# Optimization experiments

Hardware: AMD Instinct MI355X
Metric: run time of the kernel (lower is better)

Reference implementation:

```python
import jax, jax.numpy as jnp
import numpy as np

WS = 7       # window_size
SHIFT = 3    # shift_size
HEADS = 3
EPS = 1e-5


def _rel_index():
    # (2, N) coords of a WS x WS window, then pairwise relative offsets -> flat table index
    coords = np.stack(np.meshgrid(np.arange(WS), np.arange(WS), indexing='ij')).reshape(2, -1)
    rel = (coords[:, :, None] - coords[:, None, :]).transpose(1, 2, 0) + (WS - 1)  # (N,N,2)
    return jnp.asarray(rel[..., 0] * (2 * WS - 1) + rel[..., 1])  # (N,N) int


def _layernorm(x, g, b):
    mu = jnp.mean(x, axis=-1, keepdims=True)
    var = jnp.mean(jnp.square(x - mu), axis=-1, keepdims=True)
    return (x - mu) * jax.lax.rsqrt(var + EPS) * g + b


def setup_inputs() -> dict:
    key = jax.random.key(0)
    ks = jax.random.split(key, 6)
    C, HID = 96, 384
    s = 0.02
    return {
        'x': jax.random.normal(ks[0], (8, C, 224, 224), jnp.float32),
        'norm1_g': jnp.ones((C,), jnp.float32),
        'norm1_b': jnp.zeros((C,), jnp.float32),
        'qkv_w': jax.random.normal(ks[1], (C, 3 * C), jnp.float32) * s,
        'qkv_b': jnp.zeros((3 * C,), jnp.float32),
        'proj_w': jax.random.normal(ks[2], (C, C), jnp.float32) * s,
        'proj_b': jnp.zeros((C,), jnp.float32),
        'rel_bias_table': jax.random.normal(ks[3], ((2 * WS - 1) ** 2, HEADS), jnp.float32) * s,
        'norm2_g': jnp.ones((C,), jnp.float32),
        'norm2_b': jnp.zeros((C,), jnp.float32),
        'fc1_w': jax.random.normal(ks[4], (C, HID), jnp.float32) * s,
        'fc1_b': jnp.zeros((HID,), jnp.float32),
        'fc2_w': jax.random.normal(ks[5], (HID, C), jnp.float32) * s,
        'fc2_b': jnp.zeros((C,), jnp.float32),
    }


def reference(x, norm1_g, norm1_b, qkv_w, qkv_b, proj_w, proj_b,
              rel_bias_table, norm2_g, norm2_b, fc1_w, fc1_b, fc2_w, fc2_b):
    B, C, H, W = x.shape
    N = WS * WS
    dh = C // HEADS

    # norm1 over channels (tokens = flattened spatial)
    xt = x.reshape(B, C, H * W).transpose(0, 2, 1)          # (B, L, C)
    xn = _layernorm(xt, norm1_g, norm1_b)
    xs = xn.transpose(0, 2, 1).reshape(B, C, H, W)
    # H, W divisible by WS -> pad is a no-op; cyclic shift
    xs = jnp.roll(xs, (-SHIFT, -SHIFT), axis=(2, 3))

    # window partition -> (B*nW, N, C)
    xw = xs.reshape(B, C, H // WS, WS, W // WS, WS)
    xw = xw.transpose(0, 2, 4, 3, 5, 1).reshape(-1, N, C)

    # window attention with relative position bias (no shift mask, per source)
    Bw = xw.shape[0]
    qkv = (xw @ qkv_w + qkv_b).reshape(Bw, N, 3, HEADS, dh).transpose(2, 0, 3, 1, 4)
    q, k, v = qkv[0], qkv[1], qkv[2]                        # (Bw, h, N, dh)
    attn = jnp.einsum('bhnd,bhmd->bhnm', q, k) * (dh ** -0.5)
    bias = rel_bias_table[_rel_index().reshape(-1)].reshape(N, N, HEADS).transpose(2, 0, 1)
    attn = jax.nn.softmax(attn + bias, axis=-1)
    out = jnp.einsum('bhnm,bhmd->bhnd', attn, v).transpose(0, 2, 1, 3).reshape(Bw, N, C)
    out = out @ proj_w + proj_b

    # window reverse + unshift
    xr = out.reshape(B, H // WS, W // WS, WS, WS, C)
    xr = xr.transpose(0, 5, 1, 3, 2, 4).reshape(B, C, H, W)
    xr = jnp.roll(xr, (SHIFT, SHIFT), axis=(2, 3))

    x = x + xr                                              # residual 1

    # MLP branch with norm2 (exact GELU, matching torch nn.GELU default)
    xt = x.reshape(B, C, H * W).transpose(0, 2, 1)
    xn = _layernorm(xt, norm2_g, norm2_b)
    h = jax.nn.gelu(xn @ fc1_w + fc1_b, approximate=False)
    h = h @ fc2_w + fc2_b
    return x + h.transpose(0, 2, 1).reshape(B, C, H, W)
```

## Files before the change

### kernel.cpp

```cpp
#include <hip/hip_runtime.h>
#include <hip/hip_bf16.h>
#include <math.h>

#define WSZ 7
#define NTOK 49
#define CH 96
#define HIMG 224
#define WIMG 224
#define HWIMG (224*224)
#define SHIFT_ 3
#define HID 384

typedef __attribute__((ext_vector_type(8))) short bf16x8;
typedef __attribute__((ext_vector_type(4))) float f32x4;
typedef unsigned int u32;
typedef unsigned short u16;

__device__ __forceinline__ u32 pk2(float a, float b) {
    u16 ua = __builtin_bit_cast(u16, __float2bfloat16(a));
    u16 ub = __builtin_bit_cast(u16, __float2bfloat16(b));
    return (u32)ua | ((u32)ub << 16);
}
__device__ __forceinline__ float bflo(u32 u) { return __builtin_bit_cast(float, u << 16); }
__device__ __forceinline__ float bfhi(u32 u) { return __builtin_bit_cast(float, u & 0xFFFF0000u); }

union FragU { u32 w[4]; bf16x8 v; };

__device__ __forceinline__ bf16x8 regroup(u32 t0w0, u32 t0w1, u32 t1w0, u32 t1w1, int lane) {
    int sl0 = (lane & 15) + ((lane & 16) << 1);
    int sl1 = sl0 + 16;
    u32 x0 = (u32)__shfl((int)t0w0, sl0);
    u32 y0 = (u32)__shfl((int)t1w0, sl0);
    u32 x1 = (u32)__shfl((int)t0w1, sl0);
    u32 y1 = (u32)__shfl((int)t1w1, sl0);
    u32 x2 = (u32)__shfl((int)t0w0, sl1);
    u32 y2 = (u32)__shfl((int)t1w0, sl1);
    u32 x3 = (u32)__shfl((int)t0w1, sl1);
    u32 y3 = (u32)__shfl((int)t1w1, sl1);
    bool lo = lane < 32;
    FragU f;
    f.w[0] = lo ? x0 : y0;
    f.w[1] = lo ? x1 : y1;
    f.w[2] = lo ? x2 : y2;
    f.w[3] = lo ? x3 : y3;
    return f.v;
}

__device__ __forceinline__ float gelu_f(float x) {
    float x2 = x * x;
    float t  = x * (1.5957691216057308f + 0.07135481283587191f * x2);
    float e  = __expf(t);
    float r  = __builtin_amdgcn_rcpf(e + 1.0f);
    return x - x * r;
}

__global__ __launch_bounds__(256) void prep_kernel(
    const float* __restrict__ w1, const float* __restrict__ w2,
    const float* __restrict__ pw, const float* __restrict__ qw,
    __hip_bfloat16* __restrict__ ws, int n)
{
    int i = blockIdx.x * 256 + threadIdx.x;
    if (i >= n) return;
    float val = 0.f;
    if (i < 81920) {
        int ch = i / 20480, r = i - ch * 20480;
        int half = r / 10240;
        int rr = r - half * 10240;
        if (rr < 9984) {
            int row = rr / 104, col = rr - row * 104;
            if (col < 96)
                val = (half == 0) ? w1[col * HID + ch * 96 + row]
                                  : w2[(size_t)(ch * 96 + col) * CH + row];
        }
    } else if (i < 92160) {
        int r = i - 81920;
        if (r < 9984) {
            int row = r / 104, col = r - row * 104;
            if (col < 96) val = pw[col * CH + row];
        }
    } else {
        int j = i - 92160;
        int hh = j / 9984, rr = j - hh * 9984;
        int dp = rr / 104, c = rr - dp * 104;
        if (c < 96) {
            int colW = (dp < 32) ? (hh * 32 + dp)
                     : (dp < 64) ? (96 + hh * 32 + dp - 32)
                                 : (192 + hh * 32 + dp - 64);
            val = qw[c * 288 + colW];
        }
    }
    ws[i] = __float2bfloat16(val);
}

__global__ __launch_bounds__(256) void attn2_kernel(
    const float* __restrict__ x,
    const float* __restrict__ g1, const float* __restrict__ b1,
    const __hip_bfloat16* __restrict__ wsW,
    const float* __restrict__ qkv_b, const float* __restrict__ pb,
    const float* __restrict__ btab,
    __hip_bfloat16* __restrict__ projout)
{
    const int tid  = threadIdx.x;
    const int lane = tid & 63;
    const int wv   = tid >> 6;
    const int l15  = lane & 15;
    const int g    = lane >> 4;
    const int bi   = blockIdx.x;
    const int b    = bi >> 8;
    const int wh   = (bi >> 3) & 31;
    const int ww0  = (bi & 7) * 4;
    const int ww   = ww0 + wv;

    __shared__ float btabL[512];
    __shared__ __align__(16) __hip_bfloat16 slab[32][7][32];
    __shared__ __align__(16) char uniA[4][4608];

    __hip_bfloat16 (*vT)[72] = (__hip_bfloat16(*)[72])uniA[wv];
    u32* prS = (u32*)uniA[wv];

    for (int idx = tid; idx < 507; idx += 256) btabL[idx] = btab[idx];

    const int colBase = ww0 * 7 + 3;
    const int cb4 = (colBase & ~3) >> 2;
    const int a0  = colBase & 3;

    int yiA[4], scA[4]; bool realA[4];
    #pragma unroll
    for (int it = 0; it < 4; ++it) {
        int i = it * 16 + l15;
        realA[it] = i < NTOK;
        int yi = i / 7, xi = i - yi * 7;
        yiA[it] = yi; scA[it] = a0 + wv * 7 + xi;
    }

    float s0a[4] = {0.f, 0.f, 0.f, 0.f}, s1a[4] = {0.f, 0.f, 0.f, 0.f};
    FragU xf[4][3];

    for (int ks = 0; ks < 3; ++ks) {
        #pragma unroll
        for (int k = 0; k < 7; ++k) {
            int idx = tid + 256 * k;
            int c = idx / 56, rem = idx - c * 56;
            int r = rem >> 3, cf = rem & 7;
            int gr = wh * 7 + 3 + r; if (gr >= HIMG) gr -= HIMG;
            int g4 = cb4 + cf; if (g4 >= 56) g4 -= 56;
            float4 v = *(const float4*)(x + ((size_t)(b * CH + ks * 32 + c) * HIMG + gr) * WIMG + g4 * 4);
            uint2 pk;
            pk.x = pk2(v.x, v.y);
            pk.y = pk2(v.z, v.w);
            *(uint2*)&slab[c][r][cf * 4] = pk;
        }
        __syncthreads();
        #pragma unroll
        for (int it = 0; it < 4; ++it) {
            float v[8];
            #pragma unroll
            for (int t = 0; t < 8; ++t) {
                float val = realA[it] ? __bfloat162float(slab[g * 8 + t][yiA[it]][scA[it]]) : 0.f;
                v[t] = val;
                s0a[it] += val; s1a[it] += val * val;
            }
            xf[it][ks].w[0] = pk2(v[0], v[1]);
            xf[it][ks].w[1] = pk2(v[2], v[3]);
            xf[it][ks].w[2] = pk2(v[4], v[5]);
            xf[it][ks].w[3] = pk2(v[6], v[7]);
        }
        __syncthreads();
    }

    float mu4[4], rs4[4];
    #pragma unroll
    for (int it = 0; it < 4; ++it) {
        float s0 = s0a[it]; s0 += __shfl_xor(s0, 16); s0 += __shfl_xor(s0, 32);
        float s1 = s1a[it]; s1 += __shfl_xor(s1, 16); s1 += __shfl_xor(s1, 32);
        float mu = s0 * (1.0f / CH);
        mu4[it] = mu;
        rs4[it] = rsqrtf(s1 * (1.0f / CH) - mu * mu + 1e-5f);
    }
    #pragma unroll
    for (int ks = 0; ks < 3; ++ks) {
        float4 gA = *(const float4*)&g1[ks * 32 + g * 8];
        float4 gB = *(const float4*)&g1[ks * 32 + g * 8 + 4];
        float4 bA = *(const float4*)&b1[ks * 32 + g * 8];
        float4 bB = *(const float4*)&b1[ks * 32 + g * 8 + 4];
        float gg[8] = {gA.x, gA.y, gA.z, gA.w, gB.x, gB.y, gB.z, gB.w};
        float bb[8] = {bA.x, bA.y, bA.z, bA.w, bB.x, bB.y, bB.z, bB.w};
        #pragma unroll
        for (int it = 0; it < 4; ++it) {
            #pragma unroll
            for (int w = 0; w < 4; ++w) {
                u32 u = xf[it][ks].w[w];
                float lo = bflo(u), hi = bfhi(u);
                float nlo = realA[it] ? ((lo - mu4[it]) * rs4[it] * gg[2 * w]     + bb[2 * w])     : 0.f;
                float nhi = realA[it] ? ((hi - mu4[it]) * rs4[it] * gg[2 * w + 1] + bb[2 * w + 1]) : 0.f;
                xf[it][ks].w[w] = pk2(nlo, nhi);
            }
        }
    }

    const float scale = 0.17677669529663687f;
    bf16x8 aoB[3][4];

    for (int h = 0; h < 3; ++h) {
        const __hip_bfloat16* qkvTg = wsW + 92160 + h * 9984;

        float qb[2][4], kb[2][4], vb[2][4];
        #pragma unroll
        for (int dt = 0; dt < 2; ++dt)
            #pragma unroll
            for (int r = 0; r < 4; ++r) {
                int d = h * 32 + dt * 16 + g * 4 + r;
                qb[dt][r] = qkv_b[d];
                kb[dt][r] = qkv_b[96 + d];
                vb[dt][r] = qkv_b[192 + d];
            }

        u32 Qpk[2][4][2];
        #pragma unroll
        for (int dt = 0; dt < 2; ++dt) {
            const __hip_bfloat16* wr = qkvTg + (dt * 16 + l15) * 104 + g * 8;
            bf16x8 a0f = *(const bf16x8*)(wr);
            bf16x8 a1f = *(const bf16x8*)(wr + 32);
            bf16x8 a2f = *(const bf16x8*)(wr + 64);
            #pragma unroll
            for (int it = 0; it < 4; ++it) {
                f32x4 c4 = {0.f, 0.f, 0.f, 0.f};
                c4 = __builtin_amdgcn_mfma_f32_16x16x32_bf16(a0f, xf[it][0].v, c4, 0, 0, 0);
                c4 = __builtin_amdgcn_mfma_f32_16x16x32_bf16(a1f, xf[it][1].v, c4, 0, 0, 0);
                c4 = __builtin_amdgcn_mfma_f32_16x16x32_bf16(a2f, xf[it][2].v, c4, 0, 0, 0);
                Qpk[dt][it][0] = pk2(c4[0] + qb[dt][0], c4[1] + qb[dt][1]);
                Qpk[dt][it][1] = pk2(c4[2] + qb[dt][2], c4[3] + qb[dt][3]);
            }
        }
        bf16x8 QB[4];
        #pragma unroll
        for (int it = 0; it < 4; ++it)
            QB[it] = regroup(Qpk[0][it][0], Qpk[0][it][1], Qpk[1][it][0], Qpk[1][it][1], lane);

        u32 Kpk[2][4][2];
        #pragma unroll
        for (int dt = 0; dt < 2; ++dt) {
            const __hip_bfloat16* wr = qkvTg + (32 + dt * 16 + l15) * 104 + g * 8;
            bf16x8 a0f = *(const bf16x8*)(wr);
            bf16x8 a1f = *(const bf16x8*)(wr + 32);
            bf16x8 a2f = *(const bf16x8*)(wr + 64);
            #pragma unroll
            for (int it = 0; it < 4; ++it) {
                f32x4 c4 = {0.f, 0.f, 0.f, 0.f};
                c4 = __builtin_amdgcn_mfma_f32_16x16x32_bf16(a0f, xf[it][0].v, c4, 0, 0, 0);
                c4 = __builtin_amdgcn_mfma_f32_16x16x32_bf16(a1f, xf[it][1].v, c4, 0, 0, 0);
                c4 = __builtin_amdgcn_mfma_f32_16x16x32_bf16(a2f, xf[it][2].v, c4, 0, 0, 0);
                Kpk[dt][it][0] = pk2(c4[0] + kb[dt][0], c4[1] + kb[dt][1]);
                Kpk[dt][it][1] = pk2(c4[2] + kb[dt][2], c4[3] + kb[dt][3]);
            }
        }
        bf16x8 KA[4];
        #pragma unroll
        for (int it = 0; it < 4; ++it)
            KA[it] = regroup(Kpk[0][it][0], Kpk[0][it][1], Kpk[1][it][0], Kpk[1][it][1], lane);

        #pragma unroll
        for (int dt = 0; dt < 2; ++dt) {
            const __hip_bfloat16* wr = qkvTg + (64 + dt * 16 + l15) * 104 + g * 8;
            bf16x8 a0f = *(const bf16x8*)(wr);
            bf16x8 a1f = *(const bf16x8*)(wr + 32);
            bf16x8 a2f = *(const bf16x8*)(wr + 64);
            #pragma unroll
            for (int it = 0; it < 4; ++it) {
                f32x4 c4 = {0.f, 0.f, 0.f, 0.f};
                c4 = __builtin_amdgcn_mfma_f32_16x16x32_bf16(a0f, xf[it][0].v, c4, 0, 0, 0);
                c4 = __builtin_amdgcn_mfma_f32_16x16x32_bf16(a1f, xf[it][1].v, c4, 0, 0, 0);
                c4 = __builtin_amdgcn_mfma_f32_16x16x32_bf16(a2f, xf[it][2].v, c4, 0, 0, 0);
                #pragma unroll
                for (int r = 0; r < 4; ++r)
                    vT[dt * 16 + g * 4 + r][it * 16 + l15] = __float2bfloat16(c4[r] + vb[dt][r]);
            }
        }
        bf16x8 VBf[2][2];
        #pragma unroll
        for (int dt = 0; dt < 2; ++dt)
            #pragma unroll
            for (int ks = 0; ks < 2; ++ks)
                VBf[dt][ks] = *(const bf16x8*)&vT[dt * 16 + l15][ks * 32 + g * 8];

        #pragma unroll
        for (int it = 0; it < 4; ++it) {
            f32x4 SC[4];
            #pragma unroll
            for (int jt = 0; jt < 4; ++jt) {
                f32x4 z = {0.f, 0.f, 0.f, 0.f};
                SC[jt] = __builtin_amdgcn_mfma_f32_16x16x32_bf16(KA[jt], QB[it], z, 0, 0, 0);
            }
            int i = it * 16 + l15;
            int yi = i / 7, xi = i - yi * 7;
            float p[16];
            float m = -1e30f;
            #pragma unroll
            for (int jt = 0; jt < 4; ++jt)
                #pragma unroll
                for (int r = 0; r < 4; ++r) {
                    int j = jt * 16 + g * 4 + r;
                    int yj = j / 7, xj = j - yj * 7;
                    int rel = (yi - yj + 6) * 13 + (xi - xj + 6);
                    rel = rel < 0 ? 0 : (rel > 168 ? 168 : rel);
                    float s = (j < NTOK) ? (SC[jt][r] * scale + btabL[rel * 3 + h]) : -1e30f;
                    p[jt * 4 + r] = s;
                    m = fmaxf(m, s);
                }
            m = fmaxf(m, __shfl_xor(m, 16));
            m = fmaxf(m, __shfl_xor(m, 32));
            float sum = 0.f;
            #pragma unroll
            for (int q = 0; q < 16; ++q) { float e = __expf(p[q] - m); p[q] = e; sum += e; }
            sum += __shfl_xor(sum, 16);
            sum += __shfl_xor(sum, 32);
            float inv = 1.f / sum;
            u32 Ppk[4][2];
            #pragma unroll
            for (int jt = 0; jt < 4; ++jt) {
                Ppk[jt][0] = pk2(p[jt * 4 + 0] * inv, p[jt * 4 + 1] * inv);
                Ppk[jt][1] = pk2(p[jt * 4 + 2] * inv, p[jt * 4 + 3] * inv);
            }
            bf16x8 PA0 = regroup(Ppk[0][0], Ppk[0][1], Ppk[1][0], Ppk[1][1], lane);
            bf16x8 PA1 = regroup(Ppk[2][0], Ppk[2][1], Ppk[3][0], Ppk[3][1], lane);
            u32 opk[2][2];
            #pragma unroll
            for (int dt = 0; dt < 2; ++dt) {
                f32x4 o = {0.f, 0.f, 0.f, 0.f};
                o = __builtin_amdgcn_mfma_f32_16x16x32_bf16(PA0, VBf[dt][0], o, 0, 0, 0);
                o = __builtin_amdgcn_mfma_f32_16x16x32_bf16(PA1, VBf[dt][1], o, 0, 0, 0);
                opk[dt][0] = pk2(o[0], o[1]);
                opk[dt][1] = pk2(o[2], o[3]);
            }
            aoB[h][it] = regroup(opk[0][0], opk[0][1], opk[1][0], opk[1][1], lane);
        }
    }

    const __hip_bfloat16* pwTg = wsW + 81920;
    for (int it = 0; it < 4; ++it) {
        #pragma unroll
        for (int mt = 0; mt < 6; ++mt) {
            const __hip_bfloat16* wr = pwTg + (mt * 16 + l15) * 104 + g * 8;
            f32x4 cp = {0.f, 0.f, 0.f, 0.f};
            #pragma unroll
            for (int ks = 0; ks < 3; ++ks) {
                bf16x8 af = *(const bf16x8*)(wr + ks * 32);
                cp = __builtin_amdgcn_mfma_f32_16x16x32_bf16(af, aoB[ks][it], cp, 0, 0, 0);
            }
            float v0 = cp[0] + pb[mt * 16 + g * 4 + 0];
            float v1 = cp[1] + pb[mt * 16 + g * 4 + 1];
            float v2 = cp[2] + pb[mt * 16 + g * 4 + 2];
            float v3 = cp[3] + pb[mt * 16 + g * 4 + 3];
            prS[l15 * 52 + mt * 8 + g * 2 + 0] = pk2(v0, v1);
            prS[l15 * 52 + mt * 8 + g * 2 + 1] = pk2(v2, v3);
        }
        #pragma unroll
        for (int s = 0; s < 3; ++s) {
            int chunk = lane + 64 * s;
            int row = chunk / 12, q = chunk - row * 12;
            int tok = it * 16 + row;
            if (tok < NTOK) {
                int yi = tok / 7, xi = tok - yi * 7;
                int hh = wh * 7 + yi + SHIFT_; if (hh >= HIMG) hh -= HIMG;
                int wp = ww * 7 + xi + SHIFT_; if (wp >= WIMG) wp -= WIMG;
                float4 val = *(const float4*)((const char*)prS + row * 208 + q * 16);
                *(float4*)(projout + ((size_t)b * HWIMG + hh * WIMG + wp) * 96 + q * 8) = val;
            }
        }
    }
}

#define LDSTG(p0, p1, p2, s) { const float4* _s = wsrc + (s) * 1280; \
    p0 = _s[tid]; p1 = _s[tid + 512]; if (tid < 256) p2 = _s[tid + 1024]; }
#define WRSTG(p0, p1, p2, off) { float4* _d = (float4*)(SB + (off)); \
    _d[tid] = p0; _d[tid + 512] = p1; if (tid < 256) _d[tid + 1024] = p2; }

__global__ __launch_bounds__(512, 4) void mlp2_kernel(
    const float* __restrict__ x, const __hip_bfloat16* __restrict__ projout,
    const float* __restrict__ g2, const float* __restrict__ b2,
    const float* __restrict__ bb1, const float* __restrict__ bb2,
    const __hip_bfloat16* __restrict__ wsW,
    float* __restrict__ out)
{
    const int tid = threadIdx.x;
    const int lane = tid & 63, wv = tid >> 6;
    const int l15 = lane & 15, g = lane >> 4;
    const int b = blockIdx.x / 392;
    const int hw0 = (blockIdx.x % 392) * 128;
    const int tok = wv * 16 + l15;

    __shared__ __align__(16) char SB[50688];
    __shared__ float bb1S[HID];

    __hip_bfloat16 (*xnS)[104] = (__hip_bfloat16(*)[104])SB;
    __hip_bfloat16 (*wT0)[104] = (__hip_bfloat16(*)[104])SB;
    __hip_bfloat16 (*wT1)[104] = (__hip_bfloat16(*)[104])(SB + 20480);
    float* ob = (float*)SB;

    const float4* wsrc = (const float4*)wsW;
    float4 ra0, ra1, ra2, rb0, rb1, rb2;

    LDSTG(ra0, ra1, ra2, 0);

    #pragma unroll
    for (int s = 0; s < 3; ++s) {
        int chunk = tid + 512 * s;
        int row = chunk / 12, q = chunk - row * 12;
        *(float4*)&xnS[row][q * 8] =
            *(const float4*)(projout + ((size_t)b * HWIMG + hw0 + row) * 96 + q * 8);
    }
    for (int idx = tid; idx < HID; idx += 512) bb1S[idx] = bb1[idx];
    __syncthreads();

    float xr[24];
    float s0 = 0.f, s1 = 0.f;
    bf16x8 pf[3];
    #pragma unroll
    for (int ks = 0; ks < 3; ++ks)
        pf[ks] = *(const bf16x8*)&xnS[tok][ks * 32 + g * 8];
    const float* xb = x + (size_t)(b * CH) * HWIMG + hw0 + tok;
    #pragma unroll
    for (int ks = 0; ks < 3; ++ks)
        #pragma unroll
        for (int j = 0; j < 8; ++j) {
            int c = ks * 32 + g * 8 + j;
            float xv = xb[(size_t)c * HWIMG];
            float v = xv + bflo((u32)(u16)pf[ks][j]);
            xr[ks * 8 + j] = v; s0 += v; s1 += v * v;
        }
    s0 += __shfl_xor(s0, 16); s0 += __shfl_xor(s0, 32);
    s1 += __shfl_xor(s1, 16); s1 += __shfl_xor(s1, 32);
    float mu = s0 * (1.0f / CH);
    float rstd = rsqrtf(s1 * (1.0f / CH) - mu * mu + 1e-5f);

    bf16x8 xbf[3];
    #pragma unroll
    for (int ks = 0; ks < 3; ++ks) {
        float nv[8];
        #pragma unroll
        for (int j = 0; j < 8; ++j) {
            int c = ks * 32 + g * 8 + j;
            nv[j] = (xr[ks * 8 + j] - mu) * rstd * g2[c] + b2[c];
        }
        FragU f;
        f.w[0] = pk2(nv[0], nv[1]); f.w[1] = pk2(nv[2], nv[3]);
        f.w[2] = pk2(nv[4], nv[5]); f.w[3] = pk2(nv[6], nv[7]);
        xbf[ks] = f.v;
    }
    __syncthreads();

    WRSTG(ra0, ra1, ra2, 0);
    LDSTG(rb0, rb1, rb2, 1);
    __syncthreads();

    f32x4 acc[6];
    #pragma unroll
    for (int mt = 0; mt < 6; ++mt) {
        #pragma unroll
        for (int r = 0; r < 4; ++r) acc[mt][r] = bb2[mt * 16 + g * 4 + r];
    }

    #pragma unroll
    for (int ch = 0; ch < 4; ++ch) {
        u32 hpk[6][2];
        #pragma unroll
        for (int mt = 0; mt < 6; ++mt) {
            f32x4 f = {0.f, 0.f, 0.f, 0.f};
            #pragma unroll
            for (int ks = 0; ks < 3; ++ks) {
                bf16x8 af = *(const bf16x8*)&wT0[mt * 16 + l15][ks * 32 + g * 8];
                f = __builtin_amdgcn_mfma_f32_16x16x32_bf16(af, xbf[ks], f, 0, 0, 0);
            }
            float gl[4];
            #pragma unroll
            for (int r = 0; r < 4; ++r) {
                float a = f[r] + bb1S[ch * 96 + mt * 16 + g * 4 + r];
                gl[r] = gelu_f(a);
            }
            hpk[mt][0] = pk2(gl[0], gl[1]);
            hpk[mt][1] = pk2(gl[2], gl[3]);
        }
        WRSTG(rb0, rb1, rb2, 20480);
        __syncthreads();
        if (ch < 3) LDSTG(ra0, ra1, ra2, 2 * ch + 2);

        bf16x8 hf[3];
        hf[0] = regroup(hpk[0][0], hpk[0][1], hpk[1][0], hpk[1][1], lane);
        hf[1] = regroup(hpk[2][0], hpk[2][1], hpk[3][0], hpk[3][1], lane);
        hf[2] = regroup(hpk[4][0], hpk[4][1], hpk[5][0], hpk[5][1], lane);
        #pragma unroll
        for (int mt = 0; mt < 6; ++mt) {
            #pragma unroll
            for (int ks = 0; ks < 3; ++ks) {
                bf16x8 af = *(const bf16x8*)&wT1[mt * 16 + l15][ks * 32 + g * 8];
                acc[mt] = __builtin_amdgcn_mfma_f32_16x16x32_bf16(af, hf[ks], acc[mt], 0, 0, 0);
            }
        }
        if (ch < 3) WRSTG(ra0, ra1, ra2, 0);
        __syncthreads();
        if (ch < 3) LDSTG(rb0, rb1, rb2, 2 * ch + 3);
    }

    #pragma unroll
    for (int ks = 0; ks < 3; ++ks)
        #pragma unroll
        for (int j = 0; j < 8; ++j)
            ob[tok * 99 + ks * 32 + g * 8 + j] = xr[ks * 8 + j];
    __syncthreads();
    #pragma unroll
    for (int mt = 0; mt < 6; ++mt)
        #pragma unroll
        for (int r = 0; r < 4; ++r)
            ob[tok * 99 + mt * 16 + g * 4 + r] += acc[mt][r];
    __syncthreads();
    #pragma unroll
    for (int k = 0; k < 24; ++k) {
        int idx = tid + 512 * k;
        int c = idx >> 7, t = idx & 127;
        out[(size_t)(b * CH + c) * HWIMG + hw0 + t] = ob[t * 99 + c];
    }
}

__global__ __launch_bounds__(256) void attn_fb_kernel(
    const float* __restrict__ x,
    const float* __restrict__ g1, const float* __restrict__ b1,
    const float* __restrict__ qkv_w, const float* __restrict__ qkv_b,
    const float* __restrict__ proj_w, const float* __restrict__ proj_b,
    const float* __restrict__ btab,
    float* __restrict__ out)
{
    const int tid = threadIdx.x;
    const int wid = blockIdx.x;
    const int b  = wid >> 10;
    const int wh = (wid >> 5) & 31;
    const int ww = wid & 31;

    __shared__ float ao[NTOK][CH + 1];
    __shared__ __hip_bfloat16 xnb[NTOK][CH + 2];
    __shared__ float qs[NTOK][33], ks_[NTOK][33], vs[NTOK][33];
    __shared__ float ss[NTOK][NTOK + 1];
    __shared__ float mu[NTOK], rs[NTOK];

    float xreg[19];

    for (int idx = tid, k = 0; idx < NTOK * CH; idx += 256, ++k) {
        int c = idx / NTOK, n = idx % NTOK;
        int i = n / WSZ, j = n % WSZ;
        int h = wh * WSZ + i + SHIFT_; if (h >= HIMG) h -= HIMG;
        int w = ww * WSZ + j + SHIFT_; if (w >= WIMG) w -= WIMG;
        float v = x[((size_t)(b * CH + c) * HIMG + h) * WIMG + w];
        ao[n][c] = v; xreg[k] = v;
    }
    __syncthreads();
    if (tid < NTOK) {
        float s0 = 0.f, s1 = 0.f;
        for (int c = 0; c < CH; ++c) { float v = ao[tid][c]; s0 += v; s1 += v * v; }
        float m = s0 / CH;
        mu[tid] = m; rs[tid] = rsqrtf(s1 / CH - m * m + 1e-5f);
    }
    __syncthreads();
    for (int idx = tid; idx < NTOK * CH; idx += 256) {
        int c = idx / NTOK, n = idx % NTOK;
        xnb[n][c] = __float2bfloat16((ao[n][c] - mu[n]) * rs[n] * g1[c] + b1[c]);
    }
    __syncthreads();
    const float scale = 0.17677669529663687f;
    for (int hh = 0; hh < 3; ++hh) {
        for (int idx = tid; idx < 3 * 32 * NTOK; idx += 256) {
            int col = idx / NTOK, n = idx % NTOK;
            int which = col >> 5, d = col & 31;
            int gc = which * CH + hh * 32 + d;
            float acc = qkv_b[gc];
            for (int c = 0; c < CH; ++c)
                acc += __bfloat162float(xnb[n][c]) * qkv_w[c * 288 + gc];
            if (which == 0) qs[n][d] = acc;
            else if (which == 1) ks_[n][d] = acc;
            else vs[n][d] = acc;
        }
        __syncthreads();
        for (int idx = tid; idx < NTOK * NTOK; idx += 256) {
            int i = idx / NTOK, j = idx % NTOK;
            float acc = 0.f;
            for (int d = 0; d < 32; ++d) acc += qs[i][d] * ks_[j][d];
            int yi = i / WSZ, xi = i % WSZ, yj = j / WSZ, xj = j % WSZ;
            int rel = (yi - yj + 6) * 13 + (xi - xj + 6);
            ss[i][j] = acc * scale + btab[rel * 3 + hh];
        }
        __syncthreads();
        if (tid < NTOK) {
            float m = -1e30f;
            for (int j = 0; j < NTOK; ++j) m = fmaxf(m, ss[tid][j]);
            float sum = 0.f;
            for (int j = 0; j < NTOK; ++j) { float e = __expf(ss[tid][j] - m); ss[tid][j] = e; sum += e; }
            float inv = 1.f / sum;
            for (int j = 0; j < NTOK; ++j) ss[tid][j] *= inv;
        }
        __syncthreads();
        for (int idx = tid; idx < NTOK * 32; idx += 256) {
            int n = idx / 32, d = idx % 32;
            float acc = 0.f;
            for (int j = 0; j < NTOK; ++j) acc += ss[n][j] * vs[j][d];
            ao[n][hh * 32 + d] = acc;
        }
        __syncthreads();
    }
    for (int idx = tid, k = 0; idx < NTOK * CH; idx += 256, ++k) {
        int oc = idx / NTOK, n = idx % NTOK;
        int i = n / WSZ, j = n % WSZ;
        int h = wh * WSZ + i + SHIFT_; if (h >= HIMG) h -= HIMG;
        int w = ww * WSZ + j + SHIFT_; if (w >= WIMG) w -= WIMG;
        float acc = proj_b[oc];
        for (int cc = 0; cc < CH; ++cc) acc += ao[n][cc] * proj_w[cc * CH + oc];
        out[((size_t)(b * CH + oc) * HIMG + h) * WIMG + w] = xreg[k] + acc;
    }
}

__global__ __launch_bounds__(256) void mlp_fb_kernel(
    const float* __restrict__ g2, const float* __restrict__ b2,
    const float* __restrict__ w1, const float* __restrict__ bb1,
    const float* __restrict__ w2, const float* __restrict__ bb2,
    float* __restrict__ io)
{
    const int tid = threadIdx.x;
    const int b = blockIdx.x / 784;
    const int hw0 = (blockIdx.x % 784) * 64;

    __shared__ float xt[CH][64];
    __shared__ __hip_bfloat16 xn2[CH][66];
    __shared__ float hbuf[64][65];
    __shared__ float mu2[64], rs2[64];

    for (int idx = tid; idx < CH * 64; idx += 256) {
        int c = idx / 64, t = idx % 64;
        xt[c][t] = io[((size_t)(b * CH + c)) * HWIMG + hw0 + t];
    }
    __syncthreads();
    if (tid < 64) {
        float s0 = 0.f, s1 = 0.f;
        for (int c = 0; c < CH; ++c) { float v = xt[c][tid]; s0 += v; s1 += v * v; }
        float m = s0 / CH;
        mu2[tid] = m; rs2[tid] = rsqrtf(s1 / CH - m * m + 1e-5f);
    }
    __syncthreads();
    for (int idx = tid; idx < CH * 64; idx += 256) {
        int c = idx / 64, t = idx % 64;
        xn2[c][t] = __float2bfloat16((xt[c][t] - mu2[t]) * rs2[t] * g2[c] + b2[c]);
    }
    __syncthreads();
    const int tt = tid & 63, oc0 = tid >> 6;
    float acc[24];
    #pragma unroll
    for (int k = 0; k < 24; ++k) acc[k] = bb2[oc0 + 4 * k];
    for (int kc = 0; kc < HID; kc += 64) {
        for (int idx = tid; idx < 64 * 64; idx += 256) {
            int kk = idx / 64, t = idx % 64;
            float a = bb1[kc + kk];
            for (int c = 0; c < CH; ++c)
                a += __bfloat162float(xn2[c][t]) * w1[c * HID + kc + kk];
            hbuf[t][kk] = gelu_f(a);
        }
        __syncthreads();
        for (int kk = 0; kk < 64; ++kk) {
            float hv = hbuf[tt][kk];
            const float* wrow = &w2[(size_t)(kc + kk) * CH + oc0];
            #pragma unroll
            for (int k = 0; k < 24; ++k) acc[k] += hv * wrow[4 * k];
        }
        __syncthreads();
    }
    #pragma unroll
    for (int k = 0; k < 24; ++k) {
        int oc = oc0 + 4 * k;
        io[((size_t)(b * CH + oc)) * HWIMG + hw0 + tt] = xt[oc][tt] + acc[k];
    }
}

extern "C" void kernel_launch(void* const* d_in, const int* in_sizes, int n_in,
                              void* d_out, int out_size, void* d_ws, size_t ws_size,
                              hipStream_t stream) {
    const float* x    = (const float*)d_in[0];
    const float* n1g  = (const float*)d_in[1];
    const float* n1b  = (const float*)d_in[2];
    const float* qkvw = (const float*)d_in[3];
    const float* qkvb = (const float*)d_in[4];
    const float* pw   = (const float*)d_in[5];
    const float* pbv  = (const float*)d_in[6];
    const float* bt   = (const float*)d_in[7];
    const float* n2g  = (const float*)d_in[8];
    const float* n2b  = (const float*)d_in[9];
    const float* f1w  = (const float*)d_in[10];
    const float* f1b  = (const float*)d_in[11];
    const float* f2w  = (const float*)d_in[12];
    const float* f2b  = (const float*)d_in[13];
    float* out = (float*)d_out;

    const size_t FULL_NEED = 262144ull + 77070336ull;
    if (ws_size >= FULL_NEED) {
        __hip_bfloat16* wsW = (__hip_bfloat16*)d_ws;
        __hip_bfloat16* projout = (__hip_bfloat16*)((char*)d_ws + 262144);
        prep_kernel<<<477, 256, 0, stream>>>(f1w, f2w, pw, qkvw, wsW, 122112);
        attn2_kernel<<<2048, 256, 0, stream>>>(x, n1g, n1b, wsW, qkvb, pbv, bt, projout);
        mlp2_kernel<<<3136, 512, 0, stream>>>(x, projout, n2g, n2b, f1b, f2b, wsW, out);
    } else {
        attn_fb_kernel<<<8192, 256, 0, stream>>>(x, n1g, n1b, qkvw, qkvb, pw, pbv, bt, out);
        mlp_fb_kernel<<<8 * 784, 256, 0, stream>>>(n2g, n2b, f1w, f1b, f2w, f2b, out);
    }
}
```

Baseline: 486.4 us.

## Load full window slab once, fuse layernorm single pass, add MFMA wave priorities

Stages all 96 channels of the window slab into one larger LDS buffer with a single barrier, replacing three chunked load/barrier rounds. LayerNorm statistics and normalisation are now computed per token in one pass from fp32 raw values, so the bf16 repack/unpack round trip is gone. s_setprio is raised around the MFMA sections so matrix-heavy waves get issue priority. In exchange the kernel uses more LDS (about 43KB), which may reduce the number of blocks resident per CU, and raw[24] raises register pressure.

```diff
diff --git a/kernel.cpp b/kernel.cpp
--- a/kernel.cpp
+++ b/kernel.cpp
@@ -22,7 +22,6 @@
     return (u32)ua | ((u32)ub << 16);
 }
 __device__ __forceinline__ float bflo(u32 u) { return __builtin_bit_cast(float, u << 16); }
-__device__ __forceinline__ float bfhi(u32 u) { return __builtin_bit_cast(float, u & 0xFFFF0000u); }
 
 union FragU { u32 w[4]; bf16x8 v; };
 
@@ -111,92 +110,65 @@
     const int ww0  = (bi & 7) * 4;
     const int ww   = ww0 + wv;
 
-    __shared__ float btabL[512];
-    __shared__ __align__(16) __hip_bfloat16 slab[32][7][32];
-    __shared__ __align__(16) char uniA[4][4608];
-
-    __hip_bfloat16 (*vT)[72] = (__hip_bfloat16(*)[72])uniA[wv];
-    u32* prS = (u32*)uniA[wv];
+    __shared__ float btabL[507];
+    __shared__ __align__(16) char uniA[43008];
+
+    __hip_bfloat16 (*xsb)[7][32] = (__hip_bfloat16(*)[7][32])uniA;
+    __hip_bfloat16 (*vT)[72] = (__hip_bfloat16(*)[72])(uniA + wv * 4608);
+    u32* prS = (u32*)(uniA + wv * 4608);
 
     for (int idx = tid; idx < 507; idx += 256) btabL[idx] = btab[idx];
 
     const int colBase = ww0 * 7 + 3;
-    const int cb4 = (colBase & ~3) >> 2;
+    const int cA  = colBase & ~3;
+    const int cb4 = cA >> 2;
     const int a0  = colBase & 3;
-
-    int yiA[4], scA[4]; bool realA[4];
+    #pragma unroll
+    for (int k = 0; k < 21; ++k) {
+        int idx = tid + 256 * k;
+        int c = idx / 56, rem = idx - c * 56;
+        int r = rem >> 3, cf = rem & 7;
+        int gr = wh * 7 + 3 + r; if (gr >= HIMG) gr -= HIMG;
+        int g4 = cb4 + cf; if (g4 >= 56) g4 -= 56;
+        float4 v = *(const float4*)(x + ((size_t)(b * CH + c) * HIMG + gr) * WIMG + g4 * 4);
+        uint2 pk;
+        pk.x = pk2(v.x, v.y);
+        pk.y = pk2(v.z, v.w);
+        *(uint2*)&xsb[c][r][cf * 4] = pk;
+    }
+    __syncthreads();
+
+    bf16x8 xB[4][3];
     #pragma unroll
     for (int it = 0; it < 4; ++it) {
         int i = it * 16 + l15;
-        realA[it] = i < NTOK;
+        bool real = i < NTOK;
         int yi = i / 7, xi = i - yi * 7;
-        yiA[it] = yi; scA[it] = a0 + wv * 7 + xi;
-    }
-
-    float s0a[4] = {0.f, 0.f, 0.f, 0.f}, s1a[4] = {0.f, 0.f, 0.f, 0.f};
-    FragU xf[4][3];
-
-    for (int ks = 0; ks < 3; ++ks) {
-        #pragma unroll
-        for (int k = 0; k < 7; ++k) {
-            int idx = tid + 256 * k;
-            int c = idx / 56, rem = idx - c * 56;
-            int r = rem >> 3, cf = rem & 7;
-            int gr = wh * 7 + 3 + r; if (gr >= HIMG) gr -= HIMG;
-            int g4 = cb4 + cf; if (g4 >= 56) g4 -= 56;
-            float4 v = *(const float4*)(x + ((size_t)(b * CH + ks * 32 + c) * HIMG + gr) * WIMG + g4 * 4);
-            uint2 pk;
-            pk.x = pk2(v.x, v.y);
-            pk.y = pk2(v.z, v.w);
-            *(uint2*)&slab[c][r][cf * 4] = pk;
-        }
-        __syncthreads();
-        #pragma unroll
-        for (int it = 0; it < 4; ++it) {
-            float v[8];
+        int sc = a0 + wv * 7 + xi;
+        float raw[24];
+        float s0 = 0.f, s1 = 0.f;
+        #pragma unroll
+        for (int ks = 0; ks < 3; ++ks)
             #pragma unroll
             for (int t = 0; t < 8; ++t) {
-                float val = realA[it] ? __bfloat162float(slab[g * 8 + t][yiA[it]][scA[it]]) : 0.f;
-                v[t] = val;
-                s0a[it] += val; s1a[it] += val * val;
-            }
-            xf[it][ks].w[0] = pk2(v[0], v[1]);
-            xf[it][ks].w[1] = pk2(v[2], v[3]);
-            xf[it][ks].w[2] = pk2(v[4], v[5]);
-            xf[it][ks].w[3] = pk2(v[6], v[7]);
-        }
-        __syncthreads();
-    }
-
-    float mu4[4], rs4[4];
-    #pragma unroll
-    for (int it = 0; it < 4; ++it) {
-        float s0 = s0a[it]; s0 += __shfl_xor(s0, 16); s0 += __shfl_xor(s0, 32);
-        float s1 = s1a[it]; s1 += __shfl_xor(s1, 16); s1 += __shfl_xor(s1, 32);
+                int c = ks * 32 + g * 8 + t;
+                float v = real ? __bfloat162float(xsb[c][yi][sc]) : 0.f;
+                raw[ks * 8 + t] = v; s0 += v; s1 += v * v;
+            }
+        s0 += __shfl_xor(s0, 16); s0 += __shfl_xor(s0, 32);
+        s1 += __shfl_xor(s1, 16); s1 += __shfl_xor(s1, 32);
         float mu = s0 * (1.0f / CH);
-        mu4[it] = mu;
-        rs4[it] = rsqrtf(s1 * (1.0f / CH) - mu * mu + 1e-5f);
-    }
-    #pragma unroll
-    for (int ks = 0; ks < 3; ++ks) {
-        float4 gA = *(const float4*)&g1[ks * 32 + g * 8];
-        float4 gB = *(const float4*)&g1[ks * 32 + g * 8 + 4];
-        float4 bA = *(const float4*)&b1[ks * 32 + g * 8];
-        float4 bB = *(const float4*)&b1[ks * 32 + g * 8 + 4];
-        float gg[8] = {gA.x, gA.y, gA.z, gA.w, gB.x, gB.y, gB.z, gB.w};
-        float bb[8] = {bA.x, bA.y, bA.z, bA.w, bB.x, bB.y, bB.z, bB.w};
-        #pragma unroll
-        for (int it = 0; it < 4; ++it) {
-            #pragma unroll
-            for (int w = 0; w < 4; ++w) {
-                u32 u = xf[it][ks].w[w];
-                float lo = bflo(u), hi = bfhi(u);
-                float nlo = realA[it] ? ((lo - mu4[it]) * rs4[it] * gg[2 * w]     + bb[2 * w])     : 0.f;
-                float nhi = realA[it] ? ((hi - mu4[it]) * rs4[it] * gg[2 * w + 1] + bb[2 * w + 1]) : 0.f;
-                xf[it][ks].w[w] = pk2(nlo, nhi);
-            }
-        }
-    }
+        float rstd = rsqrtf(s1 * (1.0f / CH) - mu * mu + 1e-5f);
+        #pragma unroll
+        for (int ks = 0; ks < 3; ++ks)
+            #pragma unroll
+            for (int t = 0; t < 8; ++t) {
+                int c = ks * 32 + g * 8 + t;
+                float xv = real ? ((raw[ks * 8 + t] - mu) * rstd * g1[c] + b1[c]) : 0.f;
+                xB[it][ks][t] = (short)__builtin_bit_cast(u16, __float2bfloat16(xv));
+            }
+    }
+    __syncthreads();
 
     const float scale = 0.17677669529663687f;
     bf16x8 aoB[3][4];
@@ -215,6 +187,7 @@
                 vb[dt][r] = qkv_b[192 + d];
             }
 
+        __builtin_amdgcn_s_setprio(1);
         u32 Qpk[2][4][2];
         #pragma unroll
         for (int dt = 0; dt < 2; ++dt) {
@@ -225,9 +198,9 @@
             #pragma unroll
             for (int it = 0; it < 4; ++it) {
                 f32x4 c4 = {0.f, 0.f, 0.f, 0.f};
-                c4 = __builtin_amdgcn_mfma_f32_16x16x32_bf16(a0f, xf[it][0].v, c4, 0, 0, 0);
-                c4 = __builtin_amdgcn_mfma_f32_16x16x32_bf16(a1f, xf[it][1].v, c4, 0, 0, 0);
-                c4 = __builtin_amdgcn_mfma_f32_16x16x32_bf16(a2f, xf[it][2].v, c4, 0, 0, 0);
+                c4 = __builtin_amdgcn_mfma_f32_16x16x32_bf16(a0f, xB[it][0], c4, 0, 0, 0);
+                c4 = __builtin_amdgcn_mfma_f32_16x16x32_bf16(a1f, xB[it][1], c4, 0, 0, 0);
+                c4 = __builtin_amdgcn_mfma_f32_16x16x32_bf16(a2f, xB[it][2], c4, 0, 0, 0);
                 Qpk[dt][it][0] = pk2(c4[0] + qb[dt][0], c4[1] + qb[dt][1]);
                 Qpk[dt][it][1] = pk2(c4[2] + qb[dt][2], c4[3] + qb[dt][3]);
             }
@@ -247,9 +220,9 @@
             #pragma unroll
             for (int it = 0; it < 4; ++it) {
                 f32x4 c4 = {0.f, 0.f, 0.f, 0.f};
-                c4 = __builtin_amdgcn_mfma_f32_16x16x32_bf16(a0f, xf[it][0].v, c4, 0, 0, 0);
-                c4 = __builtin_amdgcn_mfma_f32_16x16x32_bf16(a1f, xf[it][1].v, c4, 0, 0, 0);
-                c4 = __builtin_amdgcn_mfma_f32_16x16x32_bf16(a2f, xf[it][2].v, c4, 0, 0, 0);
+                c4 = __builtin_amdgcn_mfma_f32_16x16x32_bf16(a0f, xB[it][0], c4, 0, 0, 0);
+                c4 = __builtin_amdgcn_mfma_f32_16x16x32_bf16(a1f, xB[it][1], c4, 0, 0, 0);
+                c4 = __builtin_amdgcn_mfma_f32_16x16x32_bf16(a2f, xB[it][2], c4, 0, 0, 0);
                 Kpk[dt][it][0] = pk2(c4[0] + kb[dt][0], c4[1] + kb[dt][1]);
                 Kpk[dt][it][1] = pk2(c4[2] + kb[dt][2], c4[3] + kb[dt][3]);
             }
@@ -268,14 +241,15 @@
             #pragma unroll
             for (int it = 0; it < 4; ++it) {
                 f32x4 c4 = {0.f, 0.f, 0.f, 0.f};
-                c4 = __builtin_amdgcn_mfma_f32_16x16x32_bf16(a0f, xf[it][0].v, c4, 0, 0, 0);
-                c4 = __builtin_amdgcn_mfma_f32_16x16x32_bf16(a1f, xf[it][1].v, c4, 0, 0, 0);
-                c4 = __builtin_amdgcn_mfma_f32_16x16x32_bf16(a2f, xf[it][2].v, c4, 0, 0, 0);
+                c4 = __builtin_amdgcn_mfma_f32_16x16x32_bf16(a0f, xB[it][0], c4, 0, 0, 0);
+                c4 = __builtin_amdgcn_mfma_f32_16x16x32_bf16(a1f, xB[it][1], c4, 0, 0, 0);
+                c4 = __builtin_amdgcn_mfma_f32_16x16x32_bf16(a2f, xB[it][2], c4, 0, 0, 0);
                 #pragma unroll
                 for (int r = 0; r < 4; ++r)
                     vT[dt * 16 + g * 4 + r][it * 16 + l15] = __float2bfloat16(c4[r] + vb[dt][r]);
             }
         }
+        __builtin_amdgcn_s_setprio(0);
         bf16x8 VBf[2][2];
         #pragma unroll
         for (int dt = 0; dt < 2; ++dt)
@@ -285,12 +259,14 @@
 
         #pragma unroll
         for (int it = 0; it < 4; ++it) {
+            __builtin_amdgcn_s_setprio(1);
             f32x4 SC[4];
             #pragma unroll
             for (int jt = 0; jt < 4; ++jt) {
                 f32x4 z = {0.f, 0.f, 0.f, 0.f};
                 SC[jt] = __builtin_amdgcn_mfma_f32_16x16x32_bf16(KA[jt], QB[it], z, 0, 0, 0);
             }
+            __builtin_amdgcn_s_setprio(0);
             int i = it * 16 + l15;
             int yi = i / 7, xi = i - yi * 7;
             float p[16];
@@ -324,6 +300,7 @@
             bf16x8 PA0 = regroup(Ppk[0][0], Ppk[0][1], Ppk[1][0], Ppk[1][1], lane);
             bf16x8 PA1 = regroup(Ppk[2][0], Ppk[2][1], Ppk[3][0], Ppk[3][1], lane);
             u32 opk[2][2];
+            __builtin_amdgcn_s_setprio(1);
             #pragma unroll
             for (int dt = 0; dt < 2; ++dt) {
                 f32x4 o = {0.f, 0.f, 0.f, 0.f};
@@ -332,12 +309,14 @@
                 opk[dt][0] = pk2(o[0], o[1]);
                 opk[dt][1] = pk2(o[2], o[3]);
             }
+            __builtin_amdgcn_s_setprio(0);
             aoB[h][it] = regroup(opk[0][0], opk[0][1], opk[1][0], opk[1][1], lane);
         }
     }
 
     const __hip_bfloat16* pwTg = wsW + 81920;
     for (int it = 0; it < 4; ++it) {
+        __builtin_amdgcn_s_setprio(1);
         #pragma unroll
         for (int mt = 0; mt < 6; ++mt) {
             const __hip_bfloat16* wr = pwTg + (mt * 16 + l15) * 104 + g * 8;
@@ -354,6 +333,7 @@
             prS[l15 * 52 + mt * 8 + g * 2 + 0] = pk2(v0, v1);
             prS[l15 * 52 + mt * 8 + g * 2 + 1] = pk2(v2, v3);
         }
+        __builtin_amdgcn_s_setprio(0);
         #pragma unroll
         for (int s = 0; s < 3; ++s) {
             int chunk = lane + 64 * s;
```

Result: faster. 406.9 us (-16.4%).
